# Kernel tuning notes

Hardware: AMD Instinct MI355X
Metric: run time of the kernel (lower is better)

Reference implementation:

```python
import jax, jax.numpy as jnp
import numpy as np

ALPHA = 50.0  # softmax temperature from __init__
EPS = 1e-12   # torch F.normalize eps


def _l2norm(v, axis):
    return v / jnp.maximum(jnp.linalg.norm(v, axis=axis, keepdims=True), EPS)


def setup_inputs() -> dict:
    key = jax.random.key(0)
    k1, k2 = jax.random.split(key)
    N, C, H, W, K = 64, 512, 32, 32, 64
    x = jax.random.normal(k1, (N, C, H, W), jnp.float32)
    # conv.weight after _init_params has shape (dim, num_clusters) = (C, K)
    conv_weight = jax.random.normal(k2, (C, K), jnp.float32) * 0.05
    conv_bias = jnp.zeros((K,), jnp.float32)
    return {"x": x, "conv_weight": conv_weight, "conv_bias": conv_bias}


def reference(x, conv_weight, conv_bias):
    N, C, H, W = x.shape
    HW = H * W
    # normalize_input=True: L2 normalize over channel dim
    xn = _l2norm(x, axis=1)
    xf = xn.reshape(N, C, HW)                      # [N, C, HW]
    # column-normalized projection weight (F.normalize(conv.weight, dim=0))
    Wn = _l2norm(conv_weight, axis=0)              # [C, K]
    # soft assignment logits: x^T Wn -> stored as [N, K, HW]
    sa_logits = jnp.einsum('nch,ck->nkh', xf, Wn)  # [N, K, HW]
    soft_assign = jax.nn.softmax((sa_logits + conv_bias[None, :, None]) * ALPHA, axis=1)
    # VLAD via two batched contractions instead of the [N,K,C,HW] residual tensor:
    # sum_h a[n,k,h] * (x[n,:,h] - W[:,k]) = (a @ x^T)[n,k,:] - (sum_h a) * W[:,k]
    vlad = jnp.einsum('nkh,nch->nkc', soft_assign, xf) \
         - soft_assign.sum(-1)[..., None] * conv_weight.T[None]   # [N, K, C]
    vlad = _l2norm(vlad, axis=2).reshape(N, -1)    # intra-norm + flatten -> [N, K*C]
    feature = jnp.transpose(xf, (0, 2, 1))         # [N, HW, C]
    return (vlad, sa_logits, feature)
```

## Files before the change

### kernel.cpp

```cpp
#include <hip/hip_runtime.h>
#include <math.h>

#define N_   64
#define C_   512
#define HW_  1024
#define K_   64
#define ALPHA_ 50.0f
#define EPS_  1e-12f

#define OUT_VLAD 0
#define OUT_SA   2097152
#define OUT_FEAT 6291456

#define WSB_WT    0
#define WSB_WNTB  131072
#define WSB_INVN  196608
#define WSB_A     458752
#define WSB_SAP   8847360
#define WSB_PART  9895936
#define PART_ELEMS 2097152

typedef __attribute__((ext_vector_type(8))) __bf16 bf16x8;
typedef __attribute__((ext_vector_type(4))) float f32x4;
typedef __attribute__((ext_vector_type(8))) unsigned short ushort8v;

__device__ inline unsigned short f2bf(float f) {
    unsigned int u = __builtin_bit_cast(unsigned int, f);
    u = (u + 0x7FFFu + ((u >> 16) & 1u)) >> 16;
    return (unsigned short)u;
}
__device__ inline f32x4 mfma16(const unsigned short* pa, const unsigned short* pb, f32x4 c) {
    bf16x8 a = *(const bf16x8*)pa;
    bf16x8 b = *(const bf16x8*)pb;
    return __builtin_amdgcn_mfma_f32_16x16x32_bf16(a, b, c, 0, 0, 0);
}

__global__ __launch_bounds__(256) void k1_weights(const float* __restrict__ W,
                                                  float* __restrict__ wT,
                                                  unsigned short* __restrict__ wnTb) {
    int k = blockIdx.x;
    int t = threadIdx.x;
    __shared__ float red[256];
    float s = 0.f;
    for (int c = t; c < C_; c += 256) { float w = W[c * K_ + k]; s += w * w; }
    red[t] = s;
    __syncthreads();
    for (int st = 128; st > 0; st >>= 1) {
        if (t < st) red[t] += red[t + st];
        __syncthreads();
    }
    float inv = 1.f / fmaxf(sqrtf(red[0]), EPS_);
    for (int c = t; c < C_; c += 256) {
        float w = W[c * K_ + k];
        wT[k * C_ + c]   = w;
        wnTb[k * C_ + c] = f2bf(w * inv);
    }
}

#define FPITCH 520
#define LSP    20
__global__ __launch_bounds__(256, 3) void k23_fused(const float* __restrict__ x,
                                                    const unsigned short* __restrict__ wnTb,
                                                    const float* __restrict__ bias,
                                                    float* __restrict__ out,
                                                    float* __restrict__ invn,
                                                    unsigned short* __restrict__ Ab,
                                                    float* __restrict__ sumA_part) {
    __shared__ alignas(16) char smraw[32768 + 128 + 16640];
    float* Xs            = (float*)smraw;
    unsigned short* Wsh  = (unsigned short*)smraw;
    float* invsh         = (float*)(smraw + 32768);
    unsigned short* FshB = (unsigned short*)(smraw + 32896);
    f32x4* red4          = (f32x4*)(smraw + 32896);
    float* Ls            = (float*)(smraw + 32896);
    float* Bz = Ls + 64 * LSP;
    float* Zm = Bz + 64;
    float* Iv = Zm + 16;
    float* Rm = Iv + 16;
    float* Rs = Rm + 288;

    int b = blockIdx.x;
    int n = b >> 6, tile = b & 63;
    int hw0 = tile << 4;
    int t = threadIdx.x;
    int l = t & 63;
    int mr = l & 15, q = l >> 4;

    const float* xb = x + (long)n * C_ * HW_ + hw0;
    int qv = t & 3, cbase = t >> 2;
    int qs = qv ^ (cbase & 3);
    f32x4 sq = (f32x4){0.f, 0.f, 0.f, 0.f};
    f32x4* Xs4 = (f32x4*)Xs;
#pragma unroll
    for (int j = 0; j < 8; ++j) {
        int c = cbase + 64 * j;
        f32x4 v = *(const f32x4*)(xb + (long)c * HW_ + qv * 4);
        sq += v * v;
        Xs4[c * 4 + qs] = v;
    }
    red4[t] = sq;
    __syncthreads();
    if (t < 128) red4[t] += red4[t + 128]; __syncthreads();
    if (t < 64)  red4[t] += red4[t + 64];  __syncthreads();
    if (t < 32)  red4[t] += red4[t + 32];  __syncthreads();
    if (t < 16)  red4[t] += red4[t + 16];  __syncthreads();
    if (t < 8)   red4[t] += red4[t + 8];   __syncthreads();
    if (t < 4)   red4[t] += red4[t + 4];   __syncthreads();
    if (t < 16) {
        float s  = ((float*)red4)[t];
        float iv = 1.f / fmaxf(sqrtf(s), EPS_);
        invsh[t] = iv;
        invn[(long)n * HW_ + hw0 + t] = iv;
    }
    __syncthreads();

    {
        float* frow = out + OUT_FEAT + ((long)n * HW_ + hw0) * C_;
        int p = t & 15, cg = t >> 4;
        float iv = invsh[p];
        int ql = p >> 2, pr = p & 3;
#pragma unroll
        for (int j = 0; j < 8; ++j) {
            int c0 = 64 * j + cg * 4;
            float f0 = Xs[(c0    ) * 16 + ((ql ^ 0) << 2) + pr] * iv;
            float f1 = Xs[(c0 + 1) * 16 + ((ql ^ 1) << 2) + pr] * iv;
            float f2 = Xs[(c0 + 2) * 16 + ((ql ^ 2) << 2) + pr] * iv;
            float f3 = Xs[(c0 + 3) * 16 + ((ql ^ 3) << 2) + pr] * iv;
            f32x4 fv = (f32x4){f0, f1, f2, f3};
            *(f32x4*)(frow + (long)p * C_ + c0) = fv;
            uint2 u;
            u.x = (unsigned)f2bf(f0) | ((unsigned)f2bf(f1) << 16);
            u.y = (unsigned)f2bf(f2) | ((unsigned)f2bf(f3) << 16);
            *(uint2*)(FshB + p * FPITCH + c0) = u;
        }
    }

    f32x4 acc[4];
#pragma unroll
    for (int j = 0; j < 4; ++j) acc[j] = (f32x4){0.f, 0.f, 0.f, 0.f};
    for (int ch = 0; ch < 4; ++ch) {
        int c0 = ch * 128;
        __syncthreads();
#pragma unroll
        for (int j = 0; j < 4; ++j) {
            int idx = j * 256 + t;
            int row = idx >> 4, sg = idx & 15;
            *(uint4*)(Wsh + row * 136 + sg * 8) =
                *(const uint4*)(wnTb + row * C_ + c0 + sg * 8);
        }
        __syncthreads();
#pragma unroll
        for (int ks = 0; ks < 4; ++ks) {
            const unsigned short* ap = FshB + mr * FPITCH + c0 + ks * 32 + q * 8;
#pragma unroll
            for (int j = 0; j < 4; ++j) {
                const unsigned short* bp = Wsh + (j * 16 + mr) * 136 + ks * 32 + q * 8;
                acc[j] = mfma16(ap, bp, acc[j]);
            }
        }
    }
    __syncthreads();

#pragma unroll
    for (int j = 0; j < 4; ++j)
#pragma unroll
        for (int r = 0; r < 4; ++r)
            Ls[(j * 16 + mr) * LSP + q * 4 + r] = acc[j][r];
    if (t < 64) Bz[t] = bias[t];
    __syncthreads();
    {
        int p = t & 15, g = t >> 4;
        float mx = -1e30f;
#pragma unroll
        for (int kk = 0; kk < 4; ++kk) {
            int kc = g * 4 + kk;
            float z = (Ls[kc * LSP + p] + Bz[kc]) * ALPHA_;
            mx = fmaxf(mx, z);
        }
        Rm[g * 18 + p] = mx;
    }
    __syncthreads();
    if (t < 16) {
        float M = -1e30f;
#pragma unroll
        for (int g = 0; g < 16; ++g) M = fmaxf(M, Rm[g * 18 + t]);
        Zm[t] = M;
    }
    __syncthreads();
    {
        int p = t & 15, g = t >> 4;
        float M = Zm[p];
        float s = 0.f;
#pragma unroll
        for (int kk = 0; kk < 4; ++kk) {
            int kc = g * 4 + kk;
            float z = (Ls[kc * LSP + p] + Bz[kc]) * ALPHA_;
            s += __expf(z - M);
        }
        Rs[g * 18 + p] = s;
    }
    __syncthreads();
    if (t < 16) {
        float S = 0.f;
#pragma unroll
        for (int g = 0; g < 16; ++g) S += Rs[g * 18 + t];
        Iv[t] = 1.f / S;
    }
    __syncthreads();

    float* sab = out + OUT_SA + (long)n * K_ * HW_ + hw0;
    unsigned short* Arow = Ab + (long)n * K_ * HW_ + hw0;
    {
        int kc = t >> 2, p0 = (t & 3) * 4;
        f32x4 v = *(f32x4*)(Ls + kc * LSP + p0);
        *(f32x4*)(sab + (long)kc * HW_ + p0) = v;
        float bz = Bz[kc];
        float a0 = __expf((v[0] + bz) * ALPHA_ - Zm[p0])     * Iv[p0];
        float a1 = __expf((v[1] + bz) * ALPHA_ - Zm[p0 + 1]) * Iv[p0 + 1];
        float a2 = __expf((v[2] + bz) * ALPHA_ - Zm[p0 + 2]) * Iv[p0 + 2];
        float a3 = __expf((v[3] + bz) * ALPHA_ - Zm[p0 + 3]) * Iv[p0 + 3];
        uint2 u;
        u.x = (unsigned)f2bf(a0) | ((unsigned)f2bf(a1) << 16);
        u.y = (unsigned)f2bf(a2) | ((unsigned)f2bf(a3) << 16);
        *(uint2*)(Arow + (long)kc * HW_ + p0) = u;
        Ls[kc * LSP + p0]     = a0;
        Ls[kc * LSP + p0 + 1] = a1;
        Ls[kc * LSP + p0 + 2] = a2;
        Ls[kc * LSP + p0 + 3] = a3;
    }
    __syncthreads();
    if (t < 64) {
        float s = 0.f;
#pragma unroll
        for (int p = 0; p < 16; ++p) s += Ls[t * LSP + p];
        sumA_part[((long)n * 64 + tile) * 64 + t] = s;
    }
}

#define K4PITCH 72
__global__ __launch_bounds__(256, 4) void k4_vlad(const float* __restrict__ x,
                                                  const float* __restrict__ invn,
                                                  const unsigned short* __restrict__ Ab,
                                                  float* __restrict__ part) {
    __shared__ float invs[512];
    __shared__ alignas(16) unsigned short Ash[64 * K4PITCH];
    __shared__ alignas(16) unsigned short Fsh[64 * K4PITCH];
    int b  = blockIdx.x;
    int n  = b >> 4;
    int r  = b & 15;
    int c_off  = (r & 7) * 64;
    int hh     = r >> 3;
    int h_base = hh * 512;
    int t = threadIdx.x;
    int l = t & 63, w = t >> 6;
    int mr = l & 15, q = l >> 4;
    int kcb = (w >> 1) * 32, cb = (w & 1) * 32;

    invs[t]       = invn[(long)n * HW_ + h_base + t];
    invs[t + 256] = invn[(long)n * HW_ + h_base + 256 + t];

    f32x4 acc[2][2];
#pragma unroll
    for (int i = 0; i < 2; ++i)
#pragma unroll
        for (int j = 0; j < 2; ++j) acc[i][j] = (f32x4){0.f, 0.f, 0.f, 0.f};

    const unsigned short* Abase = Ab + (long)n * K_ * HW_ + h_base;
    const float* xbase = x + ((long)n * C_ + c_off) * HW_ + h_base;

    for (int ch = 0; ch < 8; ++ch) {
        int h0 = ch * 64;
        __syncthreads();
#pragma unroll
        for (int j = 0; j < 2; ++j) {
            int idx = j * 256 + t;
            int row = idx >> 3, sg = idx & 7;
            *(uint4*)(Ash + row * K4PITCH + sg * 8) =
                *(const uint4*)(Abase + (long)row * HW_ + h0 + sg * 8);
        }
#pragma unroll
        for (int j = 0; j < 2; ++j) {
            int idx = j * 256 + t;
            int row = idx >> 3, sg = idx & 7;
            const float* src = xbase + (long)row * HW_ + h0 + sg * 8;
            float4 v0 = *(const float4*)src;
            float4 v1 = *(const float4*)(src + 4);
            const float* iv = invs + h0 + sg * 8;
            ushort8v pk;
            pk[0] = f2bf(v0.x * iv[0]); pk[1] = f2bf(v0.y * iv[1]);
            pk[2] = f2bf(v0.z * iv[2]); pk[3] = f2bf(v0.w * iv[3]);
            pk[4] = f2bf(v1.x * iv[4]); pk[5] = f2bf(v1.y * iv[5]);
            pk[6] = f2bf(v1.z * iv[6]); pk[7] = f2bf(v1.w * iv[7]);
            *(ushort8v*)(Fsh + row * K4PITCH + sg * 8) = pk;
        }
        __syncthreads();
#pragma unroll
        for (int ks = 0; ks < 2; ++ks) {
            int ko = ks * 32 + q * 8;
            const unsigned short* ap0 = Ash + (kcb + mr) * K4PITCH + ko;
            const unsigned short* ap1 = Ash + (kcb + 16 + mr) * K4PITCH + ko;
#pragma unroll
            for (int j = 0; j < 2; ++j) {
                const unsigned short* bp = Fsh + (cb + j * 16 + mr) * K4PITCH + ko;
                acc[0][j] = mfma16(ap0, bp, acc[0][j]);
                acc[1][j] = mfma16(ap1, bp, acc[1][j]);
            }
        }
    }
    float* pb = part + (long)hh * PART_ELEMS + (long)n * K_ * C_ + c_off;
#pragma unroll
    for (int i = 0; i < 2; ++i)
#pragma unroll
        for (int j = 0; j < 2; ++j)
#pragma unroll
            for (int rr = 0; rr < 4; ++rr) {
                int kc = kcb + i * 16 + q * 4 + rr;
                int c  = cb + j * 16 + mr;
                pb[(long)kc * C_ + c] = acc[i][j][rr];
            }
}

__global__ __launch_bounds__(256) void k5_norm(const float* __restrict__ part,
                                               const float* __restrict__ sumA_part,
                                               const float* __restrict__ wT,
                                               float* __restrict__ vlad) {
    __shared__ float red[256];
    __shared__ float sred[64];
    int row = blockIdx.x;
    int kc  = row & 63;
    int n   = row >> 6;
    int t   = threadIdx.x;
    if (t < 64) sred[t] = sumA_part[((long)n * 64 + t) * 64 + kc];
    __syncthreads();
    if (t < 16) sred[t] = sred[t] + sred[t + 16] + sred[t + 32] + sred[t + 48];
    __syncthreads();
    if (t < 4) sred[t] = sred[t] + sred[t + 4] + sred[t + 8] + sred[t + 12];
    __syncthreads();
    float sA = sred[0] + sred[1] + sred[2] + sred[3];
    long base = (long)row * C_;
    float v0, v1;
    {
        int c = t;
        float s = part[base + c] + part[PART_ELEMS + base + c];
        v0 = s - sA * wT[kc * C_ + c];
    }
    {
        int c = t + 256;
        float s = part[base + c] + part[PART_ELEMS + base + c];
        v1 = s - sA * wT[kc * C_ + c];
    }
    red[t] = v0 * v0 + v1 * v1;
    __syncthreads();
    for (int st = 128; st > 0; st >>= 1) {
        if (t < st) red[t] += red[t + st];
        __syncthreads();
    }
    float inv = 1.f / fmaxf(sqrtf(red[0]), EPS_);
    vlad[base + t]       = v0 * inv;
    vlad[base + t + 256] = v1 * inv;
}

extern "C" void kernel_launch(void* const* d_in, const int* in_sizes, int n_in,
                              void* d_out, int out_size, void* d_ws, size_t ws_size,
                              hipStream_t stream) {
    const float* x    = (const float*)d_in[0];
    const float* W    = (const float*)d_in[1];
    const float* bias = (const float*)d_in[2];
    float* out = (float*)d_out;
    char* wsb  = (char*)d_ws;

    float* wT            = (float*)(wsb + WSB_WT);
    unsigned short* wnTb = (unsigned short*)(wsb + WSB_WNTB);
    float* invn          = (float*)(wsb + WSB_INVN);
    unsigned short* Ab   = (unsigned short*)(wsb + WSB_A);
    float* sumA_part     = (float*)(wsb + WSB_SAP);
    float* part          = (float*)(wsb + WSB_PART);

    float* vlad = out + OUT_VLAD;

    hipLaunchKernelGGL(k1_weights, dim3(64),   dim3(256), 0, stream, W, wT, wnTb);
    hipLaunchKernelGGL(k23_fused,  dim3(4096), dim3(256), 0, stream, x, wnTb, bias, out, invn, Ab, sumA_part);
    hipLaunchKernelGGL(k4_vlad,    dim3(1024), dim3(256), 0, stream, x, invn, Ab, part);
    hipLaunchKernelGGL(k5_norm,    dim3(4096), dim3(256), 0, stream, part, sumA_part, wT, vlad);
}
```

Baseline: 339.0 us.

## Replace LDS staging and block reductions with register loads and wave shuffles

In the fused projection kernel, the channel-norm reduction now uses wave shuffles instead of a multi-barrier LDS tree. The weight operand is read directly from global memory into MFMA registers rather than staged through shared memory. The softmax over clusters is done in registers with cross-lane shuffles, which removes several barrier-separated LDS passes. In the VLAD kernel, the LDS tiles for A and the normalized features are removed and each lane loads its MFMA operands straight from global memory. This cuts barriers and LDS traffic, but adds redundant, less coalesced global loads per wave, with repeated reads of x and weights across waves.

```diff
diff --git a/kernel.cpp b/kernel.cpp
--- a/kernel.cpp
+++ b/kernel.cpp
@@ -29,9 +29,7 @@
     u = (u + 0x7FFFu + ((u >> 16) & 1u)) >> 16;
     return (unsigned short)u;
 }
-__device__ inline f32x4 mfma16(const unsigned short* pa, const unsigned short* pb, f32x4 c) {
-    bf16x8 a = *(const bf16x8*)pa;
-    bf16x8 b = *(const bf16x8*)pb;
+__device__ inline f32x4 mfma16(bf16x8 a, bf16x8 b, f32x4 c) {
     return __builtin_amdgcn_mfma_f32_16x16x32_bf16(a, b, c, 0, 0, 0);
 }
 
@@ -68,22 +66,17 @@
                                                     float* __restrict__ sumA_part) {
     __shared__ alignas(16) char smraw[32768 + 128 + 16640];
     float* Xs            = (float*)smraw;
-    unsigned short* Wsh  = (unsigned short*)smraw;
+    float* Lls           = (float*)smraw;
+    float* La            = Lls + 64 * LSP;
     float* invsh         = (float*)(smraw + 32768);
     unsigned short* FshB = (unsigned short*)(smraw + 32896);
     f32x4* red4          = (f32x4*)(smraw + 32896);
-    float* Ls            = (float*)(smraw + 32896);
-    float* Bz = Ls + 64 * LSP;
-    float* Zm = Bz + 64;
-    float* Iv = Zm + 16;
-    float* Rm = Iv + 16;
-    float* Rs = Rm + 288;
 
     int b = blockIdx.x;
     int n = b >> 6, tile = b & 63;
     int hw0 = tile << 4;
     int t = threadIdx.x;
-    int l = t & 63;
+    int l = t & 63, w = t >> 6;
     int mr = l & 15, q = l >> 4;
 
     const float* xb = x + (long)n * C_ * HW_ + hw0;
@@ -98,16 +91,20 @@
         sq += v * v;
         Xs4[c * 4 + qs] = v;
     }
-    red4[t] = sq;
-    __syncthreads();
-    if (t < 128) red4[t] += red4[t + 128]; __syncthreads();
-    if (t < 64)  red4[t] += red4[t + 64];  __syncthreads();
-    if (t < 32)  red4[t] += red4[t + 32];  __syncthreads();
-    if (t < 16)  red4[t] += red4[t + 16];  __syncthreads();
-    if (t < 8)   red4[t] += red4[t + 8];   __syncthreads();
-    if (t < 4)   red4[t] += red4[t + 4];   __syncthreads();
+#pragma unroll
+    for (int off = 4; off < 64; off <<= 1) {
+        sq[0] += __shfl_down(sq[0], off, 64);
+        sq[1] += __shfl_down(sq[1], off, 64);
+        sq[2] += __shfl_down(sq[2], off, 64);
+        sq[3] += __shfl_down(sq[3], off, 64);
+    }
+    if (l < 4) red4[w * 4 + l] = sq;
+    __syncthreads();
     if (t < 16) {
-        float s  = ((float*)red4)[t];
+        const float* redf = (const float*)red4;
+        int qvv = t >> 2, comp = t & 3;
+        float s = redf[(0 * 4 + qvv) * 4 + comp] + redf[(1 * 4 + qvv) * 4 + comp]
+                + redf[(2 * 4 + qvv) * 4 + comp] + redf[(3 * 4 + qvv) * 4 + comp];
         float iv = 1.f / fmaxf(sqrtf(s), EPS_);
         invsh[t] = iv;
         invn[(long)n * HW_ + hw0 + t] = iv;
@@ -134,117 +131,97 @@
             *(uint2*)(FshB + p * FPITCH + c0) = u;
         }
     }
+    __syncthreads();
 
     f32x4 acc[4];
 #pragma unroll
     for (int j = 0; j < 4; ++j) acc[j] = (f32x4){0.f, 0.f, 0.f, 0.f};
-    for (int ch = 0; ch < 4; ++ch) {
-        int c0 = ch * 128;
-        __syncthreads();
+    {
+        const unsigned short* wrow = wnTb + mr * C_;
+#pragma unroll
+        for (int ch = 0; ch < 4; ++ch) {
+#pragma unroll
+            for (int ks = 0; ks < 4; ++ks) {
+                int co = ch * 128 + ks * 32 + q * 8;
+                bf16x8 av = *(const bf16x8*)(FshB + mr * FPITCH + co);
+                bf16x8 b0 = *(const bf16x8*)(wrow + co);
+                bf16x8 b1 = *(const bf16x8*)(wrow + 16 * C_ + co);
+                bf16x8 b2 = *(const bf16x8*)(wrow + 32 * C_ + co);
+                bf16x8 b3 = *(const bf16x8*)(wrow + 48 * C_ + co);
+                acc[0] = mfma16(av, b0, acc[0]);
+                acc[1] = mfma16(av, b1, acc[1]);
+                acc[2] = mfma16(av, b2, acc[2]);
+                acc[3] = mfma16(av, b3, acc[3]);
+            }
+        }
+    }
+
+    float e[4][4], Mx[4], Sx[4], bz[4];
+#pragma unroll
+    for (int j = 0; j < 4; ++j) bz[j] = bias[j * 16 + mr];
+#pragma unroll
+    for (int r = 0; r < 4; ++r) {
+        float m = -1e30f;
 #pragma unroll
         for (int j = 0; j < 4; ++j) {
-            int idx = j * 256 + t;
-            int row = idx >> 4, sg = idx & 15;
-            *(uint4*)(Wsh + row * 136 + sg * 8) =
-                *(const uint4*)(wnTb + row * C_ + c0 + sg * 8);
-        }
-        __syncthreads();
-#pragma unroll
-        for (int ks = 0; ks < 4; ++ks) {
-            const unsigned short* ap = FshB + mr * FPITCH + c0 + ks * 32 + q * 8;
-#pragma unroll
-            for (int j = 0; j < 4; ++j) {
-                const unsigned short* bp = Wsh + (j * 16 + mr) * 136 + ks * 32 + q * 8;
-                acc[j] = mfma16(ap, bp, acc[j]);
+            float z = (acc[j][r] + bz[j]) * ALPHA_;
+            e[j][r] = z;
+            m = fmaxf(m, z);
+        }
+        m = fmaxf(m, __shfl_xor(m, 1, 64));
+        m = fmaxf(m, __shfl_xor(m, 2, 64));
+        m = fmaxf(m, __shfl_xor(m, 4, 64));
+        m = fmaxf(m, __shfl_xor(m, 8, 64));
+        Mx[r] = m;
+        float s = 0.f;
+#pragma unroll
+        for (int j = 0; j < 4; ++j) {
+            float ee = __expf(e[j][r] - m);
+            e[j][r] = ee;
+            s += ee;
+        }
+        s += __shfl_xor(s, 1, 64);
+        s += __shfl_xor(s, 2, 64);
+        s += __shfl_xor(s, 4, 64);
+        s += __shfl_xor(s, 8, 64);
+        Sx[r] = 1.f / s;
+    }
+#pragma unroll
+    for (int j = 0; j < 4; ++j) {
+        if (j == w) {
+#pragma unroll
+            for (int r = 0; r < 4; ++r) {
+                Lls[(j * 16 + mr) * LSP + q * 4 + r] = acc[j][r];
+                La [(j * 16 + mr) * LSP + q * 4 + r] = e[j][r] * Sx[r];
             }
-        }
-    }
-    __syncthreads();
-
-#pragma unroll
-    for (int j = 0; j < 4; ++j)
-#pragma unroll
-        for (int r = 0; r < 4; ++r)
-            Ls[(j * 16 + mr) * LSP + q * 4 + r] = acc[j][r];
-    if (t < 64) Bz[t] = bias[t];
-    __syncthreads();
-    {
-        int p = t & 15, g = t >> 4;
-        float mx = -1e30f;
-#pragma unroll
-        for (int kk = 0; kk < 4; ++kk) {
-            int kc = g * 4 + kk;
-            float z = (Ls[kc * LSP + p] + Bz[kc]) * ALPHA_;
-            mx = fmaxf(mx, z);
-        }
-        Rm[g * 18 + p] = mx;
-    }
-    __syncthreads();
-    if (t < 16) {
-        float M = -1e30f;
-#pragma unroll
-        for (int g = 0; g < 16; ++g) M = fmaxf(M, Rm[g * 18 + t]);
-        Zm[t] = M;
-    }
-    __syncthreads();
-    {
-        int p = t & 15, g = t >> 4;
-        float M = Zm[p];
-        float s = 0.f;
-#pragma unroll
-        for (int kk = 0; kk < 4; ++kk) {
-            int kc = g * 4 + kk;
-            float z = (Ls[kc * LSP + p] + Bz[kc]) * ALPHA_;
-            s += __expf(z - M);
-        }
-        Rs[g * 18 + p] = s;
-    }
-    __syncthreads();
-    if (t < 16) {
-        float S = 0.f;
-#pragma unroll
-        for (int g = 0; g < 16; ++g) S += Rs[g * 18 + t];
-        Iv[t] = 1.f / S;
-    }
-    __syncthreads();
-
-    float* sab = out + OUT_SA + (long)n * K_ * HW_ + hw0;
-    unsigned short* Arow = Ab + (long)n * K_ * HW_ + hw0;
-    {
+            float ps = e[j][0] * Sx[0] + e[j][1] * Sx[1] + e[j][2] * Sx[2] + e[j][3] * Sx[3];
+            ps += __shfl_xor(ps, 16, 64);
+            ps += __shfl_xor(ps, 32, 64);
+            if (q == 0)
+                sumA_part[((long)n * 64 + tile) * 64 + j * 16 + mr] = ps;
+        }
+    }
+    __syncthreads();
+
+    {
+        float* sab = out + OUT_SA + (long)n * K_ * HW_ + hw0;
+        unsigned short* Arow = Ab + (long)n * K_ * HW_ + hw0;
         int kc = t >> 2, p0 = (t & 3) * 4;
-        f32x4 v = *(f32x4*)(Ls + kc * LSP + p0);
+        f32x4 v = *(f32x4*)(Lls + kc * LSP + p0);
         *(f32x4*)(sab + (long)kc * HW_ + p0) = v;
-        float bz = Bz[kc];
-        float a0 = __expf((v[0] + bz) * ALPHA_ - Zm[p0])     * Iv[p0];
-        float a1 = __expf((v[1] + bz) * ALPHA_ - Zm[p0 + 1]) * Iv[p0 + 1];
-        float a2 = __expf((v[2] + bz) * ALPHA_ - Zm[p0 + 2]) * Iv[p0 + 2];
-        float a3 = __expf((v[3] + bz) * ALPHA_ - Zm[p0 + 3]) * Iv[p0 + 3];
+        f32x4 a = *(f32x4*)(La + kc * LSP + p0);
         uint2 u;
-        u.x = (unsigned)f2bf(a0) | ((unsigned)f2bf(a1) << 16);
-        u.y = (unsigned)f2bf(a2) | ((unsigned)f2bf(a3) << 16);
+        u.x = (unsigned)f2bf(a[0]) | ((unsigned)f2bf(a[1]) << 16);
+        u.y = (unsigned)f2bf(a[2]) | ((unsigned)f2bf(a[3]) << 16);
         *(uint2*)(Arow + (long)kc * HW_ + p0) = u;
-        Ls[kc * LSP + p0]     = a0;
-        Ls[kc * LSP + p0 + 1] = a1;
-        Ls[kc * LSP + p0 + 2] = a2;
-        Ls[kc * LSP + p0 + 3] = a3;
-    }
-    __syncthreads();
-    if (t < 64) {
-        float s = 0.f;
-#pragma unroll
-        for (int p = 0; p < 16; ++p) s += Ls[t * LSP + p];
-        sumA_part[((long)n * 64 + tile) * 64 + t] = s;
-    }
-}
-
-#define K4PITCH 72
+    }
+}
+
 __global__ __launch_bounds__(256, 4) void k4_vlad(const float* __restrict__ x,
                                                   const float* __restrict__ invn,
                                                   const unsigned short* __restrict__ Ab,
                                                   float* __restrict__ part) {
     __shared__ float invs[512];
-    __shared__ alignas(16) unsigned short Ash[64 * K4PITCH];
-    __shared__ alignas(16) unsigned short Fsh[64 * K4PITCH];
     int b  = blockIdx.x;
     int n  = b >> 4;
     int r  = b & 15;
@@ -258,6 +235,7 @@
 
     invs[t]       = invn[(long)n * HW_ + h_base + t];
     invs[t + 256] = invn[(long)n * HW_ + h_base + 256 + t];
+    __syncthreads();
 
     f32x4 acc[2][2];
 #pragma unroll
@@ -265,46 +243,38 @@
 #pragma unroll
         for (int j = 0; j < 2; ++j) acc[i][j] = (f32x4){0.f, 0.f, 0.f, 0.f};
 
-    const unsigned short* Abase = Ab + (long)n * K_ * HW_ + h_base;
-    const float* xbase = x + ((long)n * C_ + c_off) * HW_ + h_base;
+    const unsigned short* Arow0 = Ab + (long)n * K_ * HW_ + (long)(kcb + mr) * HW_ + h_base;
+    const unsigned short* Arow1 = Arow0 + 16 * HW_;
+    const float* xr0 = x + ((long)n * C_ + c_off + cb + mr) * HW_ + h_base;
+    const float* xr1 = xr0 + 16 * HW_;
 
     for (int ch = 0; ch < 8; ++ch) {
-        int h0 = ch * 64;
-        __syncthreads();
-#pragma unroll
-        for (int j = 0; j < 2; ++j) {
-            int idx = j * 256 + t;
-            int row = idx >> 3, sg = idx & 7;
-            *(uint4*)(Ash + row * K4PITCH + sg * 8) =
-                *(const uint4*)(Abase + (long)row * HW_ + h0 + sg * 8);
-        }
-#pragma unroll
-        for (int j = 0; j < 2; ++j) {
-            int idx = j * 256 + t;
-            int row = idx >> 3, sg = idx & 7;
-            const float* src = xbase + (long)row * HW_ + h0 + sg * 8;
-            float4 v0 = *(const float4*)src;
-            float4 v1 = *(const float4*)(src + 4);
-            const float* iv = invs + h0 + sg * 8;
-            ushort8v pk;
-            pk[0] = f2bf(v0.x * iv[0]); pk[1] = f2bf(v0.y * iv[1]);
-            pk[2] = f2bf(v0.z * iv[2]); pk[3] = f2bf(v0.w * iv[3]);
-            pk[4] = f2bf(v1.x * iv[4]); pk[5] = f2bf(v1.y * iv[5]);
-            pk[6] = f2bf(v1.z * iv[6]); pk[7] = f2bf(v1.w * iv[7]);
-            *(ushort8v*)(Fsh + row * K4PITCH + sg * 8) = pk;
-        }
-        __syncthreads();
 #pragma unroll
         for (int ks = 0; ks < 2; ++ks) {
-            int ko = ks * 32 + q * 8;
-            const unsigned short* ap0 = Ash + (kcb + mr) * K4PITCH + ko;
-            const unsigned short* ap1 = Ash + (kcb + 16 + mr) * K4PITCH + ko;
-#pragma unroll
-            for (int j = 0; j < 2; ++j) {
-                const unsigned short* bp = Fsh + (cb + j * 16 + mr) * K4PITCH + ko;
-                acc[0][j] = mfma16(ap0, bp, acc[0][j]);
-                acc[1][j] = mfma16(ap1, bp, acc[1][j]);
-            }
+            int ko = ch * 64 + ks * 32 + q * 8;
+            bf16x8 a0 = *(const bf16x8*)(Arow0 + ko);
+            bf16x8 a1 = *(const bf16x8*)(Arow1 + ko);
+            const float* iv = invs + ko;
+            float4 v0 = *(const float4*)(xr0 + ko);
+            float4 v1 = *(const float4*)(xr0 + ko + 4);
+            ushort8v p0;
+            p0[0] = f2bf(v0.x * iv[0]); p0[1] = f2bf(v0.y * iv[1]);
+            p0[2] = f2bf(v0.z * iv[2]); p0[3] = f2bf(v0.w * iv[3]);
+            p0[4] = f2bf(v1.x * iv[4]); p0[5] = f2bf(v1.y * iv[5]);
+            p0[6] = f2bf(v1.z * iv[6]); p0[7] = f2bf(v1.w * iv[7]);
+            bf16x8 b0 = __builtin_bit_cast(bf16x8, p0);
+            float4 v2 = *(const float4*)(xr1 + ko);
+            float4 v3 = *(const float4*)(xr1 + ko + 4);
+            ushort8v p1;
+            p1[0] = f2bf(v2.x * iv[0]); p1[1] = f2bf(v2.y * iv[1]);
+            p1[2] = f2bf(v2.z * iv[2]); p1[3] = f2bf(v2.w * iv[3]);
+            p1[4] = f2bf(v3.x * iv[4]); p1[5] = f2bf(v3.y * iv[5]);
+            p1[6] = f2bf(v3.z * iv[6]); p1[7] = f2bf(v3.w * iv[7]);
+            bf16x8 b1 = __builtin_bit_cast(bf16x8, p1);
+            acc[0][0] = mfma16(a0, b0, acc[0][0]);
+            acc[1][0] = mfma16(a1, b0, acc[1][0]);
+            acc[0][1] = mfma16(a0, b1, acc[0][1]);
+            acc[1][1] = mfma16(a1, b1, acc[1][1]);
         }
     }
     float* pb = part + (long)hh * PART_ELEMS + (long)n * K_ * C_ + c_off;
```

Result: slower. 427.7 us (+26.2%).
